# Kernel optimization log

Hardware: AMD Instinct MI355X
Metric: run time of the kernel (lower is better)

The kernel has to match this reference:

```python
import jax, jax.numpy as jnp
import numpy as np

B, IN, OUT, NC, S = 4096, 512, 512, 64, 1


def setup_inputs() -> dict:
    key = jax.random.key(0)
    k = jax.random.split(key, 5)
    x = jax.random.normal(k[0], (B, IN), dtype=jnp.float32)
    centers = jax.random.normal(k[1], (NC, IN), dtype=jnp.float32)
    log_sigma = jnp.zeros((NC,), dtype=jnp.float32)
    coeff_mean = jax.random.normal(k[2], (IN, OUT, NC), dtype=jnp.float32) * 0.05
    coeff_log_var = jnp.full((IN, OUT, NC), -5.0, dtype=jnp.float32)
    base_weight = jax.random.normal(k[3], (IN, OUT), dtype=jnp.float32) * 0.05
    eps = jax.random.normal(k[4], (S, IN, OUT, NC), dtype=jnp.float32)
    return {"x": x, "centers": centers, "log_sigma": log_sigma,
            "coeff_mean": coeff_mean, "coeff_log_var": coeff_log_var,
            "base_weight": base_weight, "eps": eps}


def reference(x, centers, log_sigma, coeff_mean, coeff_log_var, base_weight, eps):
    # RBF basis: (B, NC). Original repeats this along in_features, but the
    # einsum 'bin,ion->bo' with an i-constant basis equals rbf @ coeffs.sum(i).
    dist_sq = jnp.sum((x[:, None, :] - centers[None, :, :]) ** 2, axis=-1)  # (B, NC)
    sigma = jnp.exp(log_sigma)  # (NC,)
    rbf = jnp.exp(-dist_sq / (2.0 * sigma ** 2 + 1e-8))  # (B, NC)

    # Sampled variational coefficients, reparameterized.
    std = jnp.exp(0.5 * coeff_log_var)
    coeffs = coeff_mean + eps * std            # (S, IN, OUT, NC)
    c_sum = coeffs.sum(axis=1)                 # (S, OUT, NC): sum over in_features
    n_samples = eps.shape[0]
    rbf_out = jnp.einsum('bn,son->bo', rbf, c_sum) / n_samples  # mean over samples

    out = rbf_out + x @ base_weight

    # KL vs N(0, 1) prior (prior_scale = 1.0): log(var/prior_var) = coeff_log_var
    var = jnp.exp(coeff_log_var)
    kl = 0.5 * jnp.sum(var + coeff_mean ** 2 - 1.0 - coeff_log_var)
    return out, kl
```

## Files before the change

### kernel.cpp

```cpp
#include <hip/hip_runtime.h>
#include <hip/hip_bf16.h>

#define B_SZ  4096
#define IN_F  512
#define OUT_F 512
#define NC    64
#define PAIRS 32768
#define TOT   (IN_F * PAIRS)
#define KTOT  (IN_F + NC)
#define RCH   32

typedef __attribute__((ext_vector_type(8))) short bf16x8;
typedef __attribute__((ext_vector_type(4))) float f32x4;

static __device__ inline unsigned short f2bf(float f) {
    __hip_bfloat16 h = __float2bfloat16(f);
    return *(unsigned short*)&h;
}

__global__ __launch_bounds__(512)
void k1_partial(const float* __restrict__ cm,
                const float* __restrict__ clv,
                const float* __restrict__ eps,
                float* __restrict__ part,
                float* __restrict__ klpart,
                int S) {
    int pb = blockIdx.x & 15;
    int rc = blockIdx.x >> 4;
    int p4 = pb * 2048 + (threadIdx.x << 2);
    float Sf = (float)S;

    f32x4 s = {0.f, 0.f, 0.f, 0.f};
    float klp = 0.f;

    for (int g = 0; g < 2; ++g) {
        size_t base = (size_t)(rc * 16 + g * 8) * PAIRS + p4;
        f32x4 M[8], LV[8], ES[8];
#pragma unroll
        for (int ii = 0; ii < 8; ++ii)
            M[ii] = __builtin_nontemporal_load((const f32x4*)(cm + base + (size_t)ii * PAIRS));
#pragma unroll
        for (int ii = 0; ii < 8; ++ii)
            LV[ii] = __builtin_nontemporal_load((const f32x4*)(clv + base + (size_t)ii * PAIRS));
#pragma unroll
        for (int ii = 0; ii < 8; ++ii)
            ES[ii] = __builtin_nontemporal_load((const f32x4*)(eps + base + (size_t)ii * PAIRS));
        for (int si = 1; si < S; ++si)
#pragma unroll
            for (int ii = 0; ii < 8; ++ii) {
                f32x4 e = __builtin_nontemporal_load(
                    (const f32x4*)(eps + (size_t)si * TOT + base + (size_t)ii * PAIRS));
                ES[ii] += e;
            }

#pragma unroll
        for (int ii = 0; ii < 8; ++ii) {
            float e1x = __expf(0.5f * LV[ii].x);
            float e1y = __expf(0.5f * LV[ii].y);
            float e1z = __expf(0.5f * LV[ii].z);
            float e1w = __expf(0.5f * LV[ii].w);
            s.x += Sf * M[ii].x + ES[ii].x * e1x;
            s.y += Sf * M[ii].y + ES[ii].y * e1y;
            s.z += Sf * M[ii].z + ES[ii].z * e1z;
            s.w += Sf * M[ii].w + ES[ii].w * e1w;
            klp += (e1x*e1x + M[ii].x*M[ii].x - 1.f - LV[ii].x);
            klp += (e1y*e1y + M[ii].y*M[ii].y - 1.f - LV[ii].y);
            klp += (e1z*e1z + M[ii].z*M[ii].z - 1.f - LV[ii].z);
            klp += (e1w*e1w + M[ii].w*M[ii].w - 1.f - LV[ii].w);
        }
    }

    *(f32x4*)(part + (size_t)rc * PAIRS + p4) = s;

    for (int off = 32; off; off >>= 1)
        klp += __shfl_down(klp, off, 64);
    __shared__ float wsum[8];
    if ((threadIdx.x & 63) == 0) wsum[threadIdx.x >> 6] = klp;
    __syncthreads();
    if (threadIdx.x == 0) {
        float t = 0.f;
#pragma unroll
        for (int i = 0; i < 8; ++i) t += wsum[i];
        klpart[blockIdx.x] = t;
    }
}

__global__ __launch_bounds__(512)
void k_mid(const float* __restrict__ x,
           const float* __restrict__ centers,
           const float* __restrict__ log_sigma,
           const float* __restrict__ part,
           const float* __restrict__ klpart,
           const float* __restrict__ bw,
           unsigned short* __restrict__ rbf,
           unsigned short* __restrict__ wct,
           unsigned short* __restrict__ xbf,
           float* __restrict__ kl_out,
           float inv_S) {
    __shared__ float shbuf[16 * 8 * 64];
    int bid = blockIdx.x, t = threadIdx.x;

    if (bid < 256) {
        float (*red)[8][64] = (float (*)[8][64])shbuf;
        int n = t & 63;
        int wu = __builtin_amdgcn_readfirstlane(t >> 6);
        int b0 = bid * 16;

        float creg[64];
#pragma unroll
        for (int q = 0; q < 16; ++q) {
            float4 v = *(const float4*)(centers + (size_t)n * IN_F + wu * 64 + q * 4);
            creg[q * 4 + 0] = v.x; creg[q * 4 + 1] = v.y;
            creg[q * 4 + 2] = v.z; creg[q * 4 + 3] = v.w;
        }

        float dacc[16];
#pragma unroll
        for (int bi = 0; bi < 16; ++bi) {
            const float* xr = x + (size_t)(b0 + bi) * IN_F + wu * 64;
            float d0 = 0.f, d1 = 0.f, d2 = 0.f, d3 = 0.f;
#pragma unroll
            for (int j = 0; j < 64; j += 4) {
                float t0 = xr[j + 0] - creg[j + 0];
                float t1 = xr[j + 1] - creg[j + 1];
                float t2 = xr[j + 2] - creg[j + 2];
                float t3 = xr[j + 3] - creg[j + 3];
                d0 = fmaf(t0, t0, d0); d1 = fmaf(t1, t1, d1);
                d2 = fmaf(t2, t2, d2); d3 = fmaf(t3, t3, d3);
            }
            dacc[bi] = (d0 + d1) + (d2 + d3);
        }
#pragma unroll
        for (int bi = 0; bi < 16; ++bi)
            red[bi][wu][n] = dacc[bi];
        __syncthreads();
#pragma unroll
        for (int pass = 0; pass < 2; ++pass) {
            int idx = pass * 512 + t;
            int bi = idx >> 6, nn = idx & 63;
            float ssum = 0.f;
#pragma unroll
            for (int w = 0; w < 8; ++w) ssum += red[bi][w][nn];
            float sg  = __expf(log_sigma[nn]);
            float inv = 1.f / (2.f * sg * sg + 1e-8f);
            rbf[(size_t)(b0 + bi) * NC + nn] = f2bf(__expf(-ssum * inv));
        }
    } else if (bid < 320) {
        int p = (bid - 256) * 512 + t;
        float a0 = 0.f, a1 = 0.f, a2 = 0.f, a3 = 0.f;
#pragma unroll
        for (int r = 0; r < RCH; r += 4) {
            a0 += part[(size_t)(r + 0) * PAIRS + p];
            a1 += part[(size_t)(r + 1) * PAIRS + p];
            a2 += part[(size_t)(r + 2) * PAIRS + p];
            a3 += part[(size_t)(r + 3) * PAIRS + p];
        }
        int o = p >> 6, n = p & 63;
        wct[(size_t)o * KTOT + IN_F + n] = f2bf(((a0 + a1) + (a2 + a3)) * inv_S);
    } else if (bid < 384) {
        float* tile = shbuf;
        int bb = bid - 320;
        int bi = bb >> 3, bj = bb & 7;
        int cq = t & 15, rq = t >> 4;
#pragma unroll
        for (int rr = 0; rr < 2; ++rr) {
            int row = rq * 2 + rr;
            float4 v = *(const float4*)(bw + (size_t)(bi * 64 + row) * OUT_F + bj * 64 + cq * 4);
            *(float4*)&tile[row * 68 + cq * 4] = v;
        }
        __syncthreads();
#pragma unroll
        for (int rr = 0; rr < 2; ++rr) {
            int orow = rq * 2 + rr;
            ushort4 w;
            w.x = f2bf(tile[(cq * 4 + 0) * 68 + orow]);
            w.y = f2bf(tile[(cq * 4 + 1) * 68 + orow]);
            w.z = f2bf(tile[(cq * 4 + 2) * 68 + orow]);
            w.w = f2bf(tile[(cq * 4 + 3) * 68 + orow]);
            *(ushort4*)(wct + (size_t)(bj * 64 + orow) * KTOT + bi * 64 + cq * 4) = w;
        }
    } else if (bid == 384) {
        float v = klpart[t];
        for (int off = 32; off; off >>= 1)
            v += __shfl_down(v, off, 64);
        float* wsum = shbuf;
        if ((t & 63) == 0) wsum[t >> 6] = v;
        __syncthreads();
        if (t == 0) {
            float s = 0.f;
#pragma unroll
            for (int i = 0; i < 8; ++i) s += wsum[i];
            kl_out[0] = 0.5f * s;
        }
    } else {
        size_t base = (size_t)(bid - 385) * 32768;
#pragma unroll
        for (int q = 0; q < 16; ++q) {
            size_t off = base + q * 2048 + t * 4;
            float4 v = *(const float4*)(x + off);
            ushort4 w = {f2bf(v.x), f2bf(v.y), f2bf(v.z), f2bf(v.w)};
            *(ushort4*)(xbf + off) = w;
        }
    }
}

__global__ __launch_bounds__(256)
void k3_mfma(const unsigned short* __restrict__ xbf,
             const unsigned short* __restrict__ rbf,
             const unsigned short* __restrict__ wct,
             float* __restrict__ out) {
    __shared__ __align__(16) unsigned short As[64 * 40];
    __shared__ __align__(16) unsigned short Bs[128 * 40];
    int t = threadIdx.x;
    int bm = blockIdx.x >> 2, bn = blockIdx.x & 3;
    int b0 = bm * 64, o0 = bn * 128;
    int ar = t & 63,  as_ = t >> 6;
    int br = t & 127, bh = t >> 7;
    int lane = t & 63, wv = t >> 6;
    int fm = lane & 15, kg = lane >> 4;

    f32x4 acc[8] = {{0,0,0,0},{0,0,0,0},{0,0,0,0},{0,0,0,0},
                    {0,0,0,0},{0,0,0,0},{0,0,0,0},{0,0,0,0}};
    const int aoff = (wv * 16 + fm) * 40 + kg * 8;

    for (int it = 0; it < 16; ++it) {
        int k0 = it * 32;
        bf16x8 av = *(const bf16x8*)(xbf + (size_t)(b0 + ar) * IN_F + k0 + as_ * 8);
        bf16x8 bv0 = *(const bf16x8*)(wct + (size_t)(o0 + br) * KTOT + k0 + bh * 16);
        bf16x8 bv1 = *(const bf16x8*)(wct + (size_t)(o0 + br) * KTOT + k0 + bh * 16 + 8);
        __syncthreads();
        *(bf16x8*)&As[ar * 40 + as_ * 8]      = av;
        *(bf16x8*)&Bs[br * 40 + bh * 16]      = bv0;
        *(bf16x8*)&Bs[br * 40 + bh * 16 + 8]  = bv1;
        __syncthreads();
        bf16x8 af = *(bf16x8*)&As[aoff];
#pragma unroll
        for (int nf = 0; nf < 8; ++nf) {
            bf16x8 bfr = *(bf16x8*)&Bs[(nf * 16 + fm) * 40 + kg * 8];
            acc[nf] = __builtin_amdgcn_mfma_f32_16x16x32_bf16(af, bfr, acc[nf], 0, 0, 0);
        }
    }

    for (int it = 0; it < 2; ++it) {
        int k0 = it * 32;
        bf16x8 av = *(const bf16x8*)(rbf + (size_t)(b0 + ar) * NC + k0 + as_ * 8);
        bf16x8 bv0 = *(const bf16x8*)(wct + (size_t)(o0 + br) * KTOT + IN_F + k0 + bh * 16);
        bf16x8 bv1 = *(const bf16x8*)(wct + (size_t)(o0 + br) * KTOT + IN_F + k0 + bh * 16 + 8);
        __syncthreads();
        *(bf16x8*)&As[ar * 40 + as_ * 8]      = av;
        *(bf16x8*)&Bs[br * 40 + bh * 16]      = bv0;
        *(bf16x8*)&Bs[br * 40 + bh * 16 + 8]  = bv1;
        __syncthreads();
        bf16x8 af = *(bf16x8*)&As[aoff];
#pragma unroll
        for (int nf = 0; nf < 8; ++nf) {
            bf16x8 bfr = *(bf16x8*)&Bs[(nf * 16 + fm) * 40 + kg * 8];
            acc[nf] = __builtin_amdgcn_mfma_f32_16x16x32_bf16(af, bfr, acc[nf], 0, 0, 0);
        }
    }

#pragma unroll
    for (int nf = 0; nf < 8; ++nf)
#pragma unroll
        for (int rr = 0; rr < 4; ++rr)
            out[(size_t)(b0 + wv * 16 + kg * 4 + rr) * OUT_F + o0 + nf * 16 + fm] = acc[nf][rr];
}

extern "C" void kernel_launch(void* const* d_in, const int* in_sizes, int n_in,
                              void* d_out, int out_size, void* d_ws, size_t ws_size,
                              hipStream_t stream) {
    const float* x         = (const float*)d_in[0];
    const float* centers   = (const float*)d_in[1];
    const float* log_sigma = (const float*)d_in[2];
    const float* cm        = (const float*)d_in[3];
    const float* clv       = (const float*)d_in[4];
    const float* bw        = (const float*)d_in[5];
    const float* eps       = (const float*)d_in[6];

    float* out = (float*)d_out;
    float* kl  = out + (size_t)B_SZ * OUT_F;

    float* part   = (float*)d_ws;
    float* klpart = part + (size_t)RCH * PAIRS;
    unsigned short* wct = (unsigned short*)(klpart + 512);
    unsigned short* rbf = wct + (size_t)OUT_F * KTOT;
    unsigned short* xbf = rbf + (size_t)B_SZ * NC;

    int S = in_sizes[6] / TOT;

    k1_partial<<<512, 512, 0, stream>>>(cm, clv, eps, part, klpart, S);
    k_mid<<<449, 512, 0, stream>>>(x, centers, log_sigma, part, klpart, bw,
                                   rbf, wct, xbf, kl, 1.0f / (float)S);
    k3_mfma<<<(B_SZ / 64) * (OUT_F / 128), 256, 0, stream>>>(xbf, rbf, wct, out);
}
```

Measured before the change: 248.6 us.

## Replace partial-sum buffer with atomic accumulation and retile the MFMA GEMM

The coefficient pass now uses 1024-thread blocks that each cover 8 input rows, and accumulates per-pair sums directly into one zeroed buffer via atomicAdd. This removes the 32-row partial buffer and its separate reduction stage, and the mid kernel just converts the summed row to bf16. The GEMM switches to 64x64 output tiles with a 64-wide K step, giving twice as many blocks for better occupancy. The trade-offs are atomic contention, an extra memset launch, and more reloading of the A operand.

New measurement: 269.4 us. 8.4% more time.

```diff
diff --git a/kernel.cpp b/kernel.cpp
--- a/kernel.cpp
+++ b/kernel.cpp
@@ -8,7 +8,6 @@
 #define PAIRS 32768
 #define TOT   (IN_F * PAIRS)
 #define KTOT  (IN_F + NC)
-#define RCH   32
 
 typedef __attribute__((ext_vector_type(8))) short bf16x8;
 typedef __attribute__((ext_vector_type(4))) float f32x4;
@@ -18,69 +17,69 @@
     return *(unsigned short*)&h;
 }
 
-__global__ __launch_bounds__(512)
+__global__ __launch_bounds__(1024)
 void k1_partial(const float* __restrict__ cm,
                 const float* __restrict__ clv,
                 const float* __restrict__ eps,
-                float* __restrict__ part,
+                float* __restrict__ csum,
                 float* __restrict__ klpart,
                 int S) {
-    int pb = blockIdx.x & 15;
-    int rc = blockIdx.x >> 4;
-    int p4 = pb * 2048 + (threadIdx.x << 2);
+    int pb = blockIdx.x & 7;
+    int rc = blockIdx.x >> 3;
+    int p4 = pb * 4096 + (threadIdx.x << 2);
+    size_t base = (size_t)(rc * 8) * PAIRS + p4;
     float Sf = (float)S;
+
+    f32x4 M[8], LV[8], ES[8];
+#pragma unroll
+    for (int ii = 0; ii < 8; ++ii)
+        M[ii] = __builtin_nontemporal_load((const f32x4*)(cm + base + (size_t)ii * PAIRS));
+#pragma unroll
+    for (int ii = 0; ii < 8; ++ii)
+        LV[ii] = __builtin_nontemporal_load((const f32x4*)(clv + base + (size_t)ii * PAIRS));
+#pragma unroll
+    for (int ii = 0; ii < 8; ++ii)
+        ES[ii] = __builtin_nontemporal_load((const f32x4*)(eps + base + (size_t)ii * PAIRS));
+    for (int si = 1; si < S; ++si)
+#pragma unroll
+        for (int ii = 0; ii < 8; ++ii) {
+            f32x4 e = __builtin_nontemporal_load(
+                (const f32x4*)(eps + (size_t)si * TOT + base + (size_t)ii * PAIRS));
+            ES[ii] += e;
+        }
 
     f32x4 s = {0.f, 0.f, 0.f, 0.f};
     float klp = 0.f;
-
-    for (int g = 0; g < 2; ++g) {
-        size_t base = (size_t)(rc * 16 + g * 8) * PAIRS + p4;
-        f32x4 M[8], LV[8], ES[8];
-#pragma unroll
-        for (int ii = 0; ii < 8; ++ii)
-            M[ii] = __builtin_nontemporal_load((const f32x4*)(cm + base + (size_t)ii * PAIRS));
-#pragma unroll
-        for (int ii = 0; ii < 8; ++ii)
-            LV[ii] = __builtin_nontemporal_load((const f32x4*)(clv + base + (size_t)ii * PAIRS));
-#pragma unroll
-        for (int ii = 0; ii < 8; ++ii)
-            ES[ii] = __builtin_nontemporal_load((const f32x4*)(eps + base + (size_t)ii * PAIRS));
-        for (int si = 1; si < S; ++si)
-#pragma unroll
-            for (int ii = 0; ii < 8; ++ii) {
-                f32x4 e = __builtin_nontemporal_load(
-                    (const f32x4*)(eps + (size_t)si * TOT + base + (size_t)ii * PAIRS));
-                ES[ii] += e;
-            }
-
-#pragma unroll
-        for (int ii = 0; ii < 8; ++ii) {
-            float e1x = __expf(0.5f * LV[ii].x);
-            float e1y = __expf(0.5f * LV[ii].y);
-            float e1z = __expf(0.5f * LV[ii].z);
-            float e1w = __expf(0.5f * LV[ii].w);
-            s.x += Sf * M[ii].x + ES[ii].x * e1x;
-            s.y += Sf * M[ii].y + ES[ii].y * e1y;
-            s.z += Sf * M[ii].z + ES[ii].z * e1z;
-            s.w += Sf * M[ii].w + ES[ii].w * e1w;
-            klp += (e1x*e1x + M[ii].x*M[ii].x - 1.f - LV[ii].x);
-            klp += (e1y*e1y + M[ii].y*M[ii].y - 1.f - LV[ii].y);
-            klp += (e1z*e1z + M[ii].z*M[ii].z - 1.f - LV[ii].z);
-            klp += (e1w*e1w + M[ii].w*M[ii].w - 1.f - LV[ii].w);
-        }
-    }
-
-    *(f32x4*)(part + (size_t)rc * PAIRS + p4) = s;
+#pragma unroll
+    for (int ii = 0; ii < 8; ++ii) {
+        float e1x = __expf(0.5f * LV[ii].x);
+        float e1y = __expf(0.5f * LV[ii].y);
+        float e1z = __expf(0.5f * LV[ii].z);
+        float e1w = __expf(0.5f * LV[ii].w);
+        s.x += Sf * M[ii].x + ES[ii].x * e1x;
+        s.y += Sf * M[ii].y + ES[ii].y * e1y;
+        s.z += Sf * M[ii].z + ES[ii].z * e1z;
+        s.w += Sf * M[ii].w + ES[ii].w * e1w;
+        klp += (e1x*e1x + M[ii].x*M[ii].x - 1.f - LV[ii].x);
+        klp += (e1y*e1y + M[ii].y*M[ii].y - 1.f - LV[ii].y);
+        klp += (e1z*e1z + M[ii].z*M[ii].z - 1.f - LV[ii].z);
+        klp += (e1w*e1w + M[ii].w*M[ii].w - 1.f - LV[ii].w);
+    }
+
+    atomicAdd(&csum[p4 + 0], s.x);
+    atomicAdd(&csum[p4 + 1], s.y);
+    atomicAdd(&csum[p4 + 2], s.z);
+    atomicAdd(&csum[p4 + 3], s.w);
 
     for (int off = 32; off; off >>= 1)
         klp += __shfl_down(klp, off, 64);
-    __shared__ float wsum[8];
+    __shared__ float wsum[16];
     if ((threadIdx.x & 63) == 0) wsum[threadIdx.x >> 6] = klp;
     __syncthreads();
     if (threadIdx.x == 0) {
         float t = 0.f;
 #pragma unroll
-        for (int i = 0; i < 8; ++i) t += wsum[i];
+        for (int i = 0; i < 16; ++i) t += wsum[i];
         klpart[blockIdx.x] = t;
     }
 }
@@ -89,7 +88,7 @@
 void k_mid(const float* __restrict__ x,
            const float* __restrict__ centers,
            const float* __restrict__ log_sigma,
-           const float* __restrict__ part,
+           const float* __restrict__ csum,
            const float* __restrict__ klpart,
            const float* __restrict__ bw,
            unsigned short* __restrict__ rbf,
@@ -146,20 +145,8 @@
             rbf[(size_t)(b0 + bi) * NC + nn] = f2bf(__expf(-ssum * inv));
         }
     } else if (bid < 320) {
-        int p = (bid - 256) * 512 + t;
-        float a0 = 0.f, a1 = 0.f, a2 = 0.f, a3 = 0.f;
-#pragma unroll
-        for (int r = 0; r < RCH; r += 4) {
-            a0 += part[(size_t)(r + 0) * PAIRS + p];
-            a1 += part[(size_t)(r + 1) * PAIRS + p];
-            a2 += part[(size_t)(r + 2) * PAIRS + p];
-            a3 += part[(size_t)(r + 3) * PAIRS + p];
-        }
-        int o = p >> 6, n = p & 63;
-        wct[(size_t)o * KTOT + IN_F + n] = f2bf(((a0 + a1) + (a2 + a3)) * inv_S);
-    } else if (bid < 384) {
         float* tile = shbuf;
-        int bb = bid - 320;
+        int bb = bid - 256;
         int bi = bb >> 3, bj = bb & 7;
         int cq = t & 15, rq = t >> 4;
 #pragma unroll
@@ -179,6 +166,15 @@
             w.w = f2bf(tile[(cq * 4 + 3) * 68 + orow]);
             *(ushort4*)(wct + (size_t)(bj * 64 + orow) * KTOT + bi * 64 + cq * 4) = w;
         }
+    } else if (bid < 384) {
+        size_t base = (size_t)(bid - 320) * 32768;
+#pragma unroll
+        for (int q = 0; q < 16; ++q) {
+            size_t off = base + q * 2048 + t * 4;
+            float4 v = *(const float4*)(x + off);
+            ushort4 w = {f2bf(v.x), f2bf(v.y), f2bf(v.z), f2bf(v.w)};
+            *(ushort4*)(xbf + off) = w;
+        }
     } else if (bid == 384) {
         float v = klpart[t];
         for (int off = 32; off; off >>= 1)
@@ -193,14 +189,15 @@
             kl_out[0] = 0.5f * s;
         }
     } else {
-        size_t base = (size_t)(bid - 385) * 32768;
-#pragma unroll
-        for (int q = 0; q < 16; ++q) {
-            size_t off = base + q * 2048 + t * 4;
-            float4 v = *(const float4*)(x + off);
-            ushort4 w = {f2bf(v.x), f2bf(v.y), f2bf(v.z), f2bf(v.w)};
-            *(ushort4*)(xbf + off) = w;
-        }
+        int p4 = (bid - 385) * 2048 + t * 4;
+        float4 a = *(const float4*)(csum + p4);
+        int o = p4 >> 6, n = p4 & 63;
+        ushort4 w;
+        w.x = f2bf(a.x * inv_S);
+        w.y = f2bf(a.y * inv_S);
+        w.z = f2bf(a.z * inv_S);
+        w.w = f2bf(a.w * inv_S);
+        *(ushort4*)(wct + (size_t)o * KTOT + IN_F + n) = w;
     }
 }
 
@@ -209,58 +206,52 @@
              const unsigned short* __restrict__ rbf,
              const unsigned short* __restrict__ wct,
              float* __restrict__ out) {
-    __shared__ __align__(16) unsigned short As[64 * 40];
-    __shared__ __align__(16) unsigned short Bs[128 * 40];
+    __shared__ __align__(16) unsigned short As[64 * 72];
+    __shared__ __align__(16) unsigned short Bs[64 * 72];
     int t = threadIdx.x;
-    int bm = blockIdx.x >> 2, bn = blockIdx.x & 3;
-    int b0 = bm * 64, o0 = bn * 128;
-    int ar = t & 63,  as_ = t >> 6;
-    int br = t & 127, bh = t >> 7;
+    int bm = blockIdx.x >> 3, bn = blockIdx.x & 7;
+    int b0 = bm * 64, o0 = bn * 64;
+    int ar = t & 63, ah = t >> 6;
     int lane = t & 63, wv = t >> 6;
     int fm = lane & 15, kg = lane >> 4;
 
-    f32x4 acc[8] = {{0,0,0,0},{0,0,0,0},{0,0,0,0},{0,0,0,0},
-                    {0,0,0,0},{0,0,0,0},{0,0,0,0},{0,0,0,0}};
-    const int aoff = (wv * 16 + fm) * 40 + kg * 8;
-
-    for (int it = 0; it < 16; ++it) {
-        int k0 = it * 32;
-        bf16x8 av = *(const bf16x8*)(xbf + (size_t)(b0 + ar) * IN_F + k0 + as_ * 8);
-        bf16x8 bv0 = *(const bf16x8*)(wct + (size_t)(o0 + br) * KTOT + k0 + bh * 16);
-        bf16x8 bv1 = *(const bf16x8*)(wct + (size_t)(o0 + br) * KTOT + k0 + bh * 16 + 8);
-        __syncthreads();
-        *(bf16x8*)&As[ar * 40 + as_ * 8]      = av;
-        *(bf16x8*)&Bs[br * 40 + bh * 16]      = bv0;
-        *(bf16x8*)&Bs[br * 40 + bh * 16 + 8]  = bv1;
-        __syncthreads();
-        bf16x8 af = *(bf16x8*)&As[aoff];
-#pragma unroll
-        for (int nf = 0; nf < 8; ++nf) {
-            bf16x8 bfr = *(bf16x8*)&Bs[(nf * 16 + fm) * 40 + kg * 8];
-            acc[nf] = __builtin_amdgcn_mfma_f32_16x16x32_bf16(af, bfr, acc[nf], 0, 0, 0);
-        }
-    }
-
-    for (int it = 0; it < 2; ++it) {
-        int k0 = it * 32;
-        bf16x8 av = *(const bf16x8*)(rbf + (size_t)(b0 + ar) * NC + k0 + as_ * 8);
-        bf16x8 bv0 = *(const bf16x8*)(wct + (size_t)(o0 + br) * KTOT + IN_F + k0 + bh * 16);
-        bf16x8 bv1 = *(const bf16x8*)(wct + (size_t)(o0 + br) * KTOT + IN_F + k0 + bh * 16 + 8);
-        __syncthreads();
-        *(bf16x8*)&As[ar * 40 + as_ * 8]      = av;
-        *(bf16x8*)&Bs[br * 40 + bh * 16]      = bv0;
-        *(bf16x8*)&Bs[br * 40 + bh * 16 + 8]  = bv1;
-        __syncthreads();
-        bf16x8 af = *(bf16x8*)&As[aoff];
-#pragma unroll
-        for (int nf = 0; nf < 8; ++nf) {
-            bf16x8 bfr = *(bf16x8*)&Bs[(nf * 16 + fm) * 40 + kg * 8];
-            acc[nf] = __builtin_amdgcn_mfma_f32_16x16x32_bf16(af, bfr, acc[nf], 0, 0, 0);
-        }
-    }
-
-#pragma unroll
-    for (int nf = 0; nf < 8; ++nf)
+    f32x4 acc[4] = {{0,0,0,0},{0,0,0,0},{0,0,0,0},{0,0,0,0}};
+    const int abase = (wv * 16 + fm) * 72 + kg * 8;
+    const int soff  = ar * 72 + ah * 16;
+
+    for (int it = 0; it < 9; ++it) {
+        bf16x8 av0, av1, bv0, bv1;
+        if (it < 8) {
+            int k0 = it * 64;
+            av0 = *(const bf16x8*)(xbf + (size_t)(b0 + ar) * IN_F + k0 + ah * 16);
+            av1 = *(const bf16x8*)(xbf + (size_t)(b0 + ar) * IN_F + k0 + ah * 16 + 8);
+            bv0 = *(const bf16x8*)(wct + (size_t)(o0 + ar) * KTOT + k0 + ah * 16);
+            bv1 = *(const bf16x8*)(wct + (size_t)(o0 + ar) * KTOT + k0 + ah * 16 + 8);
+        } else {
+            av0 = *(const bf16x8*)(rbf + (size_t)(b0 + ar) * NC + ah * 16);
+            av1 = *(const bf16x8*)(rbf + (size_t)(b0 + ar) * NC + ah * 16 + 8);
+            bv0 = *(const bf16x8*)(wct + (size_t)(o0 + ar) * KTOT + IN_F + ah * 16);
+            bv1 = *(const bf16x8*)(wct + (size_t)(o0 + ar) * KTOT + IN_F + ah * 16 + 8);
+        }
+        __syncthreads();
+        *(bf16x8*)&As[soff]     = av0;
+        *(bf16x8*)&As[soff + 8] = av1;
+        *(bf16x8*)&Bs[soff]     = bv0;
+        *(bf16x8*)&Bs[soff + 8] = bv1;
+        __syncthreads();
+        bf16x8 af0 = *(bf16x8*)&As[abase];
+        bf16x8 af1 = *(bf16x8*)&As[abase + 32];
+#pragma unroll
+        for (int nf = 0; nf < 4; ++nf) {
+            bf16x8 b0f = *(bf16x8*)&Bs[(nf * 16 + fm) * 72 + kg * 8];
+            acc[nf] = __builtin_amdgcn_mfma_f32_16x16x32_bf16(af0, b0f, acc[nf], 0, 0, 0);
+            bf16x8 b1f = *(bf16x8*)&Bs[(nf * 16 + fm) * 72 + 32 + kg * 8];
+            acc[nf] = __builtin_amdgcn_mfma_f32_16x16x32_bf16(af1, b1f, acc[nf], 0, 0, 0);
+        }
+    }
+
+#pragma unroll
+    for (int nf = 0; nf < 4; ++nf)
 #pragma unroll
         for (int rr = 0; rr < 4; ++rr)
             out[(size_t)(b0 + wv * 16 + kg * 4 + rr) * OUT_F + o0 + nf * 16 + fm] = acc[nf][rr];
@@ -280,16 +271,17 @@
     float* out = (float*)d_out;
     float* kl  = out + (size_t)B_SZ * OUT_F;
 
-    float* part   = (float*)d_ws;
-    float* klpart = part + (size_t)RCH * PAIRS;
+    float* csum   = (float*)d_ws;
+    float* klpart = csum + PAIRS;
     unsigned short* wct = (unsigned short*)(klpart + 512);
     unsigned short* rbf = wct + (size_t)OUT_F * KTOT;
     unsigned short* xbf = rbf + (size_t)B_SZ * NC;
 
     int S = in_sizes[6] / TOT;
 
-    k1_partial<<<512, 512, 0, stream>>>(cm, clv, eps, part, klpart, S);
-    k_mid<<<449, 512, 0, stream>>>(x, centers, log_sigma, part, klpart, bw,
+    hipMemsetAsync(csum, 0, PAIRS * sizeof(float), stream);
+    k1_partial<<<512, 1024, 0, stream>>>(cm, clv, eps, csum, klpart, S);
+    k_mid<<<401, 512, 0, stream>>>(x, centers, log_sigma, csum, klpart, bw,
                                    rbf, wct, xbf, kl, 1.0f / (float)S);
-    k3_mfma<<<(B_SZ / 64) * (OUT_F / 128), 256, 0, stream>>>(xbf, rbf, wct, out);
-}
+    k3_mfma<<<(B_SZ / 64) * (OUT_F / 64), 256, 0, stream>>>(xbf, rbf, wct, out);
+}
```
